# Kernel optimization log

Measured on AMD Instinct MI355X. Metric: run time of the kernel, lower is better.

Reference implementation:

```python
import jax, jax.numpy as jnp
import numpy as np

V, D, DI, S, B, NI = 32000, 1024, 768, 512, 8, 197
EPS = 1e-5

def _ln(x, g, b):
    m = jnp.mean(x, axis=-1, keepdims=True)
    v = jnp.var(x, axis=-1, keepdims=True)
    return (x - m) * jax.lax.rsqrt(v + EPS) * g + b

def _pos_enc(seq_len, d):
    pos = np.arange(seq_len)[:, None].astype(np.float32)
    i = np.arange(0, d, 2).astype(np.float32)
    ang = pos / np.power(10000.0, i / d)
    pe = np.zeros((seq_len, d), dtype=np.float32)
    pe[:, 0::2] = np.sin(ang)
    pe[:, 1::2] = np.cos(ang)
    return jnp.asarray(pe)

def setup_inputs() -> dict:
    key = jax.random.key(0)
    ks = jax.random.split(key, 24)
    def rn(k, shape, scale=0.02):
        return jax.random.normal(k, shape, dtype=jnp.float32) * scale
    return {
        'tokens': jax.random.randint(ks[0], (B, S), 0, V),
        'img_emb': jax.random.normal(ks[1], (B, NI, DI), dtype=jnp.float32),
        'emb_table': rn(ks[2], (V, D), 1.0),
        'Wq1': rn(ks[3], (D, D)), 'bq1': jnp.zeros((D,), jnp.float32),
        'Wk1': rn(ks[4], (D, D)), 'bk1': jnp.zeros((D,), jnp.float32),
        'Wv1': rn(ks[5], (D, D)), 'bv1': jnp.zeros((D,), jnp.float32),
        'g1': jnp.ones((D,), jnp.float32), 'b1': jnp.zeros((D,), jnp.float32),
        'Wq2': rn(ks[6], (D, D)), 'bq2': jnp.zeros((D,), jnp.float32),
        'Wk2': rn(ks[7], (DI, D)), 'bk2': jnp.zeros((D,), jnp.float32),
        'Wv2': rn(ks[8], (DI, D)), 'bv2': jnp.zeros((D,), jnp.float32),
        'g2': jnp.ones((D,), jnp.float32), 'b2': jnp.zeros((D,), jnp.float32),
        'Wp': rn(ks[9], (D, V)), 'bp': jnp.zeros((V,), jnp.float32),
    }

def _forward(tokens, img_emb, emb_table, Wq1, bq1, Wk1, bk1, Wv1, bv1, g1, b1,
             Wq2, bq2, Wk2, bk2, Wv2, bv2, g2, b2, Wp, bp):
    scale = 1.0 / jnp.sqrt(jnp.float32(D))
    x = emb_table[tokens] + _pos_enc(S, D)[None]  # [B,S,D]
    # masked (causal) self-attention
    Q = x @ Wq1 + bq1
    K = x @ Wk1 + bk1
    Vv = x @ Wv1 + bv1
    attn = jnp.einsum('bqd,bkd->bqk', Q, K) * scale
    causal = jnp.tril(jnp.ones((S, S), dtype=bool))
    attn = jnp.where(causal[None], attn, -jnp.inf)
    A = jax.nn.softmax(attn, axis=-1)
    x = _ln(A @ Vv + x, g1, b1)
    # cross-attention over image tokens
    Q2 = x @ Wq2 + bq2
    K2 = img_emb @ Wk2 + bk2
    V2 = img_emb @ Wv2 + bv2
    A2 = jax.nn.softmax(jnp.einsum('bqd,bkd->bqk', Q2, K2) * scale, axis=-1)
    x = _ln(A2 @ V2 + x, g2, b2)
    # vocab projection (note: Decoder.forward never calls self.ff)
    return x @ Wp + bp  # [B,S,V]

def reference(tokens, img_emb, emb_table, Wq1, bq1, Wk1, bk1, Wv1, bv1, g1, b1,
              Wq2, bq2, Wk2, bk2, Wv2, bv2, g2, b2, Wp, bp):
    return _forward(tokens, img_emb, emb_table, Wq1, bq1, Wk1, bk1, Wv1, bv1, g1, b1,
                    Wq2, bq2, Wk2, bk2, Wv2, bv2, g2, b2, Wp, bp)
```

## Files before the change

kernel.cpp:

```cpp
#include <hip/hip_runtime.h>
#include <hip/hip_bf16.h>


#define DEV __device__ __forceinline__

typedef __bf16 bf16x8 __attribute__((ext_vector_type(8)));
typedef float f32x4 __attribute__((ext_vector_type(4)));
typedef unsigned int u32;
typedef __hip_bfloat16 bf16;

DEV void llds16(const void* g, void* l) {
  __builtin_amdgcn_global_load_lds((const __attribute__((address_space(1))) u32*)g,
                                   (__attribute__((address_space(3))) u32*)l, 16, 0, 0);
}

DEV float wredsum(float v){
#pragma unroll
  for (int o = 32; o; o >>= 1) v += __shfl_xor(v, o, 64);
  return v;
}
DEV float wredmax(float v){
#pragma unroll
  for (int o = 32; o; o >>= 1) v = fmaxf(v, __shfl_xor(v, o, 64));
  return v;
}

DEV float b2f(unsigned short x){ return __uint_as_float((u32)x << 16); }

DEV void store_out(float* p, float v){ *p = v; }
DEV void store_out(bf16* p, float v){ *p = __float2bfloat16(v); }

template<typename OutT>
__global__ __launch_bounds__(512, 1) void gemm256_kernel(
    const bf16* __restrict__ A, const bf16* __restrict__ Bt, OutT* __restrict__ C,
    const float* __restrict__ bias, int M, int N, int K, int lda, int ldb, int ldc)
{
  __shared__ alignas(16) char lds[131072];
  const int tid  = threadIdx.x;
  const int wave = tid >> 6, lane = tid & 63;
  const int lo = lane & 15, hi = lane >> 4;
  const int hi2 = hi ^ ((lo >> 1) & 3);
  const int wr = wave >> 2, wc = wave & 3;
  const int koff = (((lane & 3) ^ ((lane >> 3) & 3)) << 3);

  const int nbx = M >> 8;
  const int nwg = nbx * (N >> 8);
  int id = blockIdx.x;
  int g = (nwg & 7) ? id : ((id & 7) * (nwg >> 3) + (id >> 3));
  const int row0 = (g % nbx) * 256, col0 = (g / nbx) * 256;
  const int NT = K >> 5;
  const int srow = lane >> 2;

  auto stageA = [&](int t) {
    char* base = lds + (t & 3) * 32768;
    const int kk = (t << 5) + koff;
#pragma unroll
    for (int j = 0; j < 2; j++) {
      const int seg = j * 8 + wave;
      llds16(A + (long)(row0 + seg * 16 + srow) * lda + kk, base + seg * 1024);
    }
  };
  auto stageB = [&](int t) {
    char* base = lds + (t & 3) * 32768 + 16384;
    const int kk = (t << 5) + koff;
#pragma unroll
    for (int j = 0; j < 2; j++) {
      const int seg = j * 8 + wave;
      llds16(Bt + (long)(col0 + seg * 16 + srow) * ldb + kk, base + seg * 1024);
    }
  };

  f32x4 acc[8][4] = {};

  stageA(0); stageB(0);
  stageA(1); stageB(1);
  stageA(2); stageB(2);
  asm volatile("s_waitcnt vmcnt(8)" ::: "memory");
  __builtin_amdgcn_s_barrier();
  asm volatile("" ::: "memory");

  for (int t = 0; t < NT; t++) {
    char* As = lds + (t & 3) * 32768;
    char* Bs = As + 16384;
    bf16x8 af[4], bfv[4];
#pragma unroll
    for (int m = 0; m < 4; m++)
      af[m] = *(const bf16x8*)(As + ((wr * 128 + m * 16 + lo) << 6) + (hi2 << 4));
#pragma unroll
    for (int n = 0; n < 4; n++)
      bfv[n] = *(const bf16x8*)(Bs + ((wc * 64 + n * 16 + lo) << 6) + (hi2 << 4));
    if (t + 3 < NT) stageA(t + 3);
    __builtin_amdgcn_s_setprio(1);
#pragma unroll
    for (int m = 0; m < 4; m++)
#pragma unroll
      for (int n = 0; n < 4; n++)
        acc[m][n] = __builtin_amdgcn_mfma_f32_16x16x32_bf16(af[m], bfv[n], acc[m][n], 0, 0, 0);
    __builtin_amdgcn_s_setprio(0);
    asm volatile("" ::: "memory");
    __builtin_amdgcn_s_barrier();
    asm volatile("" ::: "memory");
#pragma unroll
    for (int m = 0; m < 4; m++)
      af[m] = *(const bf16x8*)(As + ((wr * 128 + (m + 4) * 16 + lo) << 6) + (hi2 << 4));
    if (t + 3 < NT) stageB(t + 3);
    __builtin_amdgcn_s_setprio(1);
#pragma unroll
    for (int m = 0; m < 4; m++)
#pragma unroll
      for (int n = 0; n < 4; n++)
        acc[m + 4][n] = __builtin_amdgcn_mfma_f32_16x16x32_bf16(af[m], bfv[n], acc[m + 4][n], 0, 0, 0);
    __builtin_amdgcn_s_setprio(0);
    if (t < NT - 3)       asm volatile("s_waitcnt vmcnt(8)" ::: "memory");
    else if (t == NT - 3) asm volatile("s_waitcnt vmcnt(4)" ::: "memory");
    else                  asm volatile("s_waitcnt vmcnt(0)" ::: "memory");
    __builtin_amdgcn_s_barrier();
    asm volatile("" ::: "memory");
  }

#pragma unroll
  for (int m = 0; m < 8; m++) {
    const int r = row0 + wr * 128 + m * 16 + hi * 4;
#pragma unroll
    for (int n = 0; n < 4; n++) {
      const int c = col0 + wc * 64 + n * 16 + lo;
      const float bb = bias ? bias[c] : 0.0f;
#pragma unroll
      for (int j = 0; j < 4; j++)
        store_out(&C[(long)(r + j) * ldc + c], acc[m][n][j] + bb);
    }
  }
}

template<typename OutT>
__global__ __launch_bounds__(256) void gemm_bt_kernel(
    const bf16* __restrict__ A, const bf16* __restrict__ Bt, OutT* __restrict__ C,
    const float* __restrict__ bias, int M, int N, int K,
    int lda, int ldb, int ldc, long sA, long sB, long sC, int tri, int kcausal)
{
  A  += (long)blockIdx.z * sA;
  Bt += (long)blockIdx.z * sB;
  C  += (long)blockIdx.z * sC;
  __shared__ alignas(16) char lds[32768];
  int bx = blockIdx.x, by = blockIdx.y;
  if (tri) { int t = blockIdx.x, i = 0; while (t > i) { t -= i + 1; i++; } bx = i; by = t; }
  const int tid = threadIdx.x;
  const int wave = tid >> 6, lane = tid & 63;
  const int lo = lane & 15, hi = lane >> 4;
  const int hi2 = hi ^ ((lo >> 1) & 3);
  const int wr = wave >> 1, wc = wave & 1;
  const int row0 = bx * 128, col0 = by * 128;
  const int srow  = lane >> 2;
  const int skoff = (((lane & 3) ^ ((lane >> 3) & 3)) << 3);
  const int Keff = kcausal ? (K < row0 + 128 ? K : row0 + 128) : K;
  const int NT = Keff >> 5;

  auto stage = [&](int t) {
    char* base = lds + (t & 1) * 16384;
    const int kk = (t << 5) + skoff;
#pragma unroll
    for (int c = 0; c < 2; ++c) {
      const int seg = c*4 + wave;
      int ra = row0 + seg*16 + srow; ra = ra < M ? ra : M-1;
      llds16(A + (long)ra*lda + kk, base + seg*1024);
      int rb = col0 + seg*16 + srow; rb = rb < N ? rb : N-1;
      llds16(Bt + (long)rb*ldb + kk, base + 8192 + seg*1024);
    }
  };

  f32x4 acc[4][4] = {};

  stage(0);
  asm volatile("s_waitcnt vmcnt(0)" ::: "memory");
  __builtin_amdgcn_s_barrier();
  __builtin_amdgcn_sched_barrier(0);

  for (int t = 0; t < NT; t++) {
    const char* As = lds + (t & 1) * 16384;
    const char* Bs = As + 8192;
    if (t + 1 < NT) stage(t + 1);
    bf16x8 af[4], bfv[4];
#pragma unroll
    for (int m = 0; m < 4; m++)
      af[m] = *(const bf16x8*)(As + ((wr*64 + m*16 + lo) << 6) + (hi2 << 4));
#pragma unroll
    for (int n = 0; n < 4; n++)
      bfv[n] = *(const bf16x8*)(Bs + ((wc*64 + n*16 + lo) << 6) + (hi2 << 4));
    __builtin_amdgcn_s_setprio(1);
#pragma unroll
    for (int m = 0; m < 4; m++)
#pragma unroll
      for (int n = 0; n < 4; n++)
        acc[m][n] = __builtin_amdgcn_mfma_f32_16x16x32_bf16(af[m], bfv[n], acc[m][n], 0, 0, 0);
    __builtin_amdgcn_s_setprio(0);
    __builtin_amdgcn_sched_barrier(0);
    asm volatile("s_waitcnt vmcnt(0)" ::: "memory");
    __builtin_amdgcn_sched_barrier(0);
    __builtin_amdgcn_s_barrier();
    __builtin_amdgcn_sched_barrier(0);
  }

#pragma unroll
  for (int m = 0; m < 4; m++) {
    const int rbase = row0 + wr*64 + m*16 + hi*4;
#pragma unroll
    for (int n = 0; n < 4; n++) {
      const int cc = col0 + wc*64 + n*16 + lo;
      if (cc >= N) continue;
      const float bb = bias ? bias[cc] : 0.0f;
#pragma unroll
      for (int j = 0; j < 4; j++) {
        const int rr = rbase + j;
        if (rr < M) store_out(&C[(long)rr*ldc + cc], acc[m][n][j] + bb);
      }
    }
  }
}

__global__ __launch_bounds__(256) void wprep4_kernel(
    const float* W0, const float* W1, const float* W2, const float* W3,
    bf16* T0, bf16* T1, bf16* T2, bf16* T3, int K, int N)
{
  const int z = blockIdx.z;
  const float* W = z == 0 ? W0 : z == 1 ? W1 : z == 2 ? W2 : W3;
  bf16* T = z == 0 ? T0 : z == 1 ? T1 : z == 2 ? T2 : T3;
  __shared__ bf16 t[32][33];
  const int k0 = blockIdx.x * 32, n0 = blockIdx.y * 32;
  const int tx = threadIdx.x & 31, ty = threadIdx.x >> 5;
#pragma unroll
  for (int i = 0; i < 4; i++)
    t[ty + i*8][tx] = __float2bfloat16(W[(long)(k0 + ty + i*8)*N + n0 + tx]);
  __syncthreads();
#pragma unroll
  for (int i = 0; i < 4; i++)
    T[(long)(n0 + ty + i*8)*K + k0 + tx] = t[tx][ty + i*8];
}

__global__ __launch_bounds__(256) void transpose_pad_kernel(
    const bf16* __restrict__ in, bf16* __restrict__ out,
    int R, int Cc, int inLD, int outLD, long inBatch, long outBatch)
{
  in  += (long)blockIdx.z * inBatch;
  out += (long)blockIdx.z * outBatch;
  __shared__ bf16 t[32][33];
  const int r0 = blockIdx.x * 32, c0 = blockIdx.y * 32;
  const int tx = threadIdx.x & 31, ty = threadIdx.x >> 5;
#pragma unroll
  for (int i = 0; i < 4; i++) {
    const int r = r0 + ty + i*8;
    bf16 v = __float2bfloat16(0.0f);
    if (r < R) v = in[(long)r*inLD + c0 + tx];
    t[ty + i*8][tx] = v;
  }
  __syncthreads();
#pragma unroll
  for (int i = 0; i < 4; i++) {
    const int oc = r0 + tx;
    const int orow = c0 + ty + i*8;
    if (oc < outLD) out[(long)orow*outLD + oc] = t[tx][ty + i*8];
  }
}

__global__ __launch_bounds__(256) void concat_bias_kernel(
    const float* a, const float* b, const float* c, int n1, int n2, int n3, float* out)
{
  const int i = blockIdx.x * 256 + threadIdx.x;
  if (i >= n1 + n2 + n3) return;
  out[i] = i < n1 ? a[i] : (i < n1 + n2 ? b[i - n1] : c[i - n1 - n2]);
}

__global__ __launch_bounds__(256) void embed_kernel(
    const int* __restrict__ tok, const float* __restrict__ tbl,
    bf16* __restrict__ xb)
{
  const int row = blockIdx.x;
  const int s = row & 511;
  const float pos = (float)s;
  const float* te = tbl + (long)tok[row] * 1024;
  const int d0 = threadIdx.x * 4;
  float4 v = *(const float4*)(te + d0);
  float o[4] = {v.x, v.y, v.z, v.w};
#pragma unroll
  for (int k = 0; k < 4; k++) {
    const int d = d0 + k;
    const int i2 = d & ~1;
    const float ang = pos * exp2f((float)i2 * -0.0129762816f);
    o[k] += (d & 1) ? __cosf(ang) : __sinf(ang);
  }
  bf16 ob[4];
#pragma unroll
  for (int k = 0; k < 4; k++) ob[k] = __float2bfloat16(o[k]);
  *(ushort4*)((unsigned short*)xb + (long)row*1024 + d0) = *(ushort4*)ob;
}

__global__ __launch_bounds__(256) void cvt_bf16_kernel(const float* __restrict__ in, bf16* __restrict__ out, long n)
{
  long i = (long)blockIdx.x * blockDim.x + threadIdx.x;
  if (i < n) out[i] = __float2bfloat16(in[i]);
}

__global__ __launch_bounds__(64) void softmax_causal_kernel(
    const float* __restrict__ Sc, bf16* __restrict__ P)
{
  const int row = blockIdx.x;
  const int q = row & 511;
  const float* srow = Sc + (long)row * 512;
  bf16* prow = P + (long)row * 512;
  const int lane = threadIdx.x;
  const float scale = 0.03125f;
  float mx = -1e30f;
  for (int j = lane; j <= q; j += 64) mx = fmaxf(mx, srow[j]);
  mx = wredmax(mx);
  float sum = 0.0f;
  for (int j = lane; j <= q; j += 64) sum += expf((srow[j] - mx) * scale);
  sum = wredsum(sum);
  const float inv = 1.0f / sum;
  for (int j = lane; j < 512; j += 64) {
    float p = (j <= q) ? expf((srow[j] - mx) * scale) * inv : 0.0f;
    prow[j] = __float2bfloat16(p);
  }
}

__global__ __launch_bounds__(64) void softmax_cross_kernel(
    const float* __restrict__ Sc, bf16* __restrict__ P)
{
  const int row = blockIdx.x;
  const float* srow = Sc + (long)row * 224;
  bf16* prow = P + (long)row * 224;
  const int lane = threadIdx.x;
  const float scale = 0.03125f;
  float mx = -1e30f;
  for (int j = lane; j < 197; j += 64) mx = fmaxf(mx, srow[j]);
  mx = wredmax(mx);
  float sum = 0.0f;
  for (int j = lane; j < 197; j += 64) sum += expf((srow[j] - mx) * scale);
  sum = wredsum(sum);
  const float inv = 1.0f / sum;
  for (int j = lane; j < 224; j += 64) {
    float p = (j < 197) ? expf((srow[j] - mx) * scale) * inv : 0.0f;
    prow[j] = __float2bfloat16(p);
  }
}

__global__ __launch_bounds__(256) void add_ln_kernel(
    const bf16* __restrict__ Acc, const bf16* __restrict__ Res,
    const float* __restrict__ g, const float* __restrict__ b,
    bf16* __restrict__ outb)
{
  const int row = blockIdx.x;
  const unsigned short* a = (const unsigned short*)Acc + (long)row * 1024;
  const unsigned short* r = (const unsigned short*)Res + (long)row * 1024;
  const int d0 = threadIdx.x * 4;
  ushort4 av = *(const ushort4*)(a + d0);
  ushort4 rv = *(const ushort4*)(r + d0);
  float vals[4] = { b2f(av.x) + b2f(rv.x), b2f(av.y) + b2f(rv.y),
                    b2f(av.z) + b2f(rv.z), b2f(av.w) + b2f(rv.w) };
  float s = vals[0] + vals[1] + vals[2] + vals[3];
  float ss = vals[0]*vals[0] + vals[1]*vals[1] + vals[2]*vals[2] + vals[3]*vals[3];
  s = wredsum(s); ss = wredsum(ss);
  __shared__ float sh[8];
  const int wave = threadIdx.x >> 6, lane = threadIdx.x & 63;
  if (lane == 0) { sh[wave] = s; sh[wave+4] = ss; }
  __syncthreads();
  s  = sh[0] + sh[1] + sh[2] + sh[3];
  ss = sh[4] + sh[5] + sh[6] + sh[7];
  const float mean = s * (1.0f/1024.0f);
  const float var  = ss * (1.0f/1024.0f) - mean*mean;
  const float inv  = rsqrtf(var + 1e-5f);
  bf16 ob[4];
#pragma unroll
  for (int i = 0; i < 4; i++) {
    const int d = d0 + i;
    ob[i] = __float2bfloat16((vals[i] - mean) * inv * g[d] + b[d]);
  }
  *(ushort4*)((unsigned short*)outb + (long)row*1024 + d0) = *(ushort4*)ob;
}

extern "C" void kernel_launch(void* const* d_in, const int* in_sizes, int n_in,
                              void* d_out, int out_size, void* d_ws, size_t ws_size,
                              hipStream_t stream) {
  const int*   tokens = (const int*)  d_in[0];
  const float* img    = (const float*)d_in[1];
  const float* emb    = (const float*)d_in[2];
  const float* Wq1    = (const float*)d_in[3];
  const float* bq1    = (const float*)d_in[4];
  const float* Wk1    = (const float*)d_in[5];
  const float* bk1    = (const float*)d_in[6];
  const float* Wv1    = (const float*)d_in[7];
  const float* bv1    = (const float*)d_in[8];
  const float* g1     = (const float*)d_in[9];
  const float* b1     = (const float*)d_in[10];
  const float* Wq2    = (const float*)d_in[11];
  const float* bq2    = (const float*)d_in[12];
  const float* Wk2    = (const float*)d_in[13];
  const float* bk2    = (const float*)d_in[14];
  const float* Wv2    = (const float*)d_in[15];
  const float* bv2    = (const float*)d_in[16];
  const float* g2     = (const float*)d_in[17];
  const float* b2     = (const float*)d_in[18];
  const float* Wp     = (const float*)d_in[19];
  const float* bp     = (const float*)d_in[20];
  float* out = (float*)d_out;

  const int B = 8, S = 512, D = 1024, DI = 768, NI = 197, NIP = 224, V = 32000;
  const int M = B * S;
  const int MI = B * NI;

  char* ws = (char*)d_ws;
  size_t off = 0;
  auto alloc = [&](size_t bytes) -> char* {
    char* p = ws + off; off += (bytes + 255) & ~(size_t)255; return p;
  };
  bf16* Wq1t = (bf16*)alloc((size_t)D*D*2);
  bf16* Wk1t = (bf16*)alloc((size_t)D*D*2);
  bf16* Wv1t = (bf16*)alloc((size_t)D*D*2);
  bf16* Wq2t = (bf16*)alloc((size_t)D*D*2);
  bf16* Wk2t = (bf16*)alloc((size_t)D*DI*2);
  bf16* Wv2t = (bf16*)alloc((size_t)D*DI*2);
  bf16* Wpt  = (bf16*)alloc((size_t)V*D*2);
  float* bqkv= (float*)alloc((size_t)3*D*4);
  float* bkv2= (float*)alloc((size_t)2*D*4);
  bf16*  xb  = (bf16*) alloc((size_t)M*D*2);
  bf16*  imgb= (bf16*) alloc((size_t)MI*DI*2);
  bf16*  QKV = (bf16*) alloc((size_t)M*3*D*2);
  bf16*  Vt  = (bf16*) alloc((size_t)M*D*2);
  float* sc1 = (float*)alloc((size_t)B*S*S*4);
  bf16*  P1  = (bf16*) alloc((size_t)B*S*S*2);
  bf16*  ao1 = (bf16*) alloc((size_t)M*D*2);
  bf16*  x2b = (bf16*) alloc((size_t)M*D*2);
  bf16*  Q2  = (bf16*) alloc((size_t)M*D*2);
  bf16*  KV2 = (bf16*) alloc((size_t)MI*2*D*2);
  bf16*  V2t = (bf16*) alloc((size_t)B*D*NIP*2);
  float* sc2 = (float*)alloc((size_t)B*S*NIP*4);
  bf16*  P2  = (bf16*) alloc((size_t)B*S*NIP*2);
  bf16*  ao2 = (bf16*) alloc((size_t)M*D*2);
  bf16*  x3b = (bf16*) alloc((size_t)M*D*2);
  (void)ws_size; (void)in_sizes; (void)n_in; (void)out_size;

  wprep4_kernel<<<dim3(D/32,  D/32, 4), 256, 0, stream>>>(Wq1, Wk1, Wv1, Wq2, Wq1t, Wk1t, Wv1t, Wq2t, D, D);
  wprep4_kernel<<<dim3(DI/32, D/32, 2), 256, 0, stream>>>(Wk2, Wv2, nullptr, nullptr, Wk2t, Wv2t, nullptr, nullptr, DI, D);
  wprep4_kernel<<<dim3(D/32,  V/32, 1), 256, 0, stream>>>(Wp, nullptr, nullptr, nullptr, Wpt, nullptr, nullptr, nullptr, D, V);
  concat_bias_kernel<<<(3*D+255)/256, 256, 0, stream>>>(bq1, bk1, bv1, D, D, D, bqkv);
  concat_bias_kernel<<<(2*D+255)/256, 256, 0, stream>>>(bk2, bv2, nullptr, D, D, 0, bkv2);

  embed_kernel<<<M, 256, 0, stream>>>(tokens, emb, xb);
  {
    long n = (long)MI * DI;
    cvt_bf16_kernel<<<(int)((n + 255)/256), 256, 0, stream>>>(img, imgb, n);
  }

  auto gemmF = [&](const bf16* A, const bf16* Bt, float* C, const float* bias,
                   int m, int n, int k, int lda, int ldb, int ldc,
                   long sA, long sB, long sC, int batch) {
    dim3 g((m+127)/128, (n+127)/128, batch);
    gemm_bt_kernel<float><<<g, 256, 0, stream>>>(A, Bt, C, bias, m, n, k, lda, ldb, ldc, sA, sB, sC, 0, 0);
  };
  auto gemmB = [&](const bf16* A, const bf16* Bt, bf16* C, const float* bias,
                   int m, int n, int k, int lda, int ldb, int ldc,
                   long sA, long sB, long sC, int batch) {
    dim3 g((m+127)/128, (n+127)/128, batch);
    gemm_bt_kernel<bf16><<<g, 256, 0, stream>>>(A, Bt, C, bias, m, n, k, lda, ldb, ldc, sA, sB, sC, 0, 0);
  };

  gemm256_kernel<bf16><<<dim3((M/256)*(3*D/256)), 512, 0, stream>>>(
      xb, Wq1t, QKV, bqkv, M, 3*D, D, D, D, 3*D);
  transpose_pad_kernel<<<dim3(S/32, D/32, B), 256, 0, stream>>>(
      QKV + 2*D, Vt, S, D, 3*D, S, (long)S*3*D, (long)D*S);
  gemm_bt_kernel<float><<<dim3(10, 1, B), 256, 0, stream>>>(
      QKV, QKV + D, sc1, nullptr, S, S, D, 3*D, 3*D, S,
      (long)S*3*D, (long)S*3*D, (long)S*S, 1, 0);
  softmax_causal_kernel<<<M, 64, 0, stream>>>(sc1, P1);
  gemm_bt_kernel<bf16><<<dim3(S/128, D/128, B), 256, 0, stream>>>(
      P1, Vt, ao1, nullptr, S, D, S, S, S, D,
      (long)S*S, (long)D*S, (long)S*D, 0, 1);
  add_ln_kernel<<<M, 256, 0, stream>>>(ao1, xb, g1, b1, x2b);

  gemm256_kernel<bf16><<<dim3((M/256)*(D/256)), 512, 0, stream>>>(
      x2b, Wq2t, Q2, bq2, M, D, D, D, D, D);
  gemmB(imgb, Wk2t, KV2, bkv2, MI, 2*D, DI, DI, DI, 2*D, 0, 0, 0, 1);
  transpose_pad_kernel<<<dim3((NIP+31)/32, D/32, B), 256, 0, stream>>>(
      KV2 + D, V2t, NI, D, 2*D, NIP, (long)NI*2*D, (long)D*NIP);
  gemmF(Q2, KV2, sc2, nullptr, S, NI, D, D, 2*D, NIP, (long)S*D, (long)NI*2*D, (long)S*NIP, B);
  softmax_cross_kernel<<<M, 64, 0, stream>>>(sc2, P2);
  gemmB(P2, V2t, ao2, nullptr, S, D, NIP, NIP, NIP, D, (long)S*NIP, (long)D*NIP, (long)S*D, B);
  add_ln_kernel<<<M, 256, 0, stream>>>(ao2, x2b, g2, b2, x3b);

  gemm256_kernel<float><<<dim3((M/256)*(V/256)), 512, 0, stream>>>(
      x3b, Wpt, out, bp, M, V, D, D, D, V);
}
```

Before: 655.8 us.

## Restructure 256x256 GEMM into BK=64 double-buffered quadrant-staged pipeline

Rewrites the main 256x256 GEMM mainloop to use a K-tile of 64 with two 64KB LDS slots instead of four 32-wide slots. Each tile's loads are split into four quarter stages that are interleaved with four MFMA quadrants, and an 8-way XOR swizzle is used for the 128-byte rows. The aim is to raise the MFMA work done per barrier and per LDS read, and to overlap global-to-LDS traffic more finely with compute. In exchange it adds many more barriers per iteration. The loop also assumes K is a multiple of 128, which could break for other shapes, and the tight LDS double-buffering reuse ordering carries a correctness risk.

```diff
diff --git a/kernel.cpp b/kernel.cpp
--- a/kernel.cpp
+++ b/kernel.cpp
@@ -30,92 +30,104 @@
 DEV void store_out(float* p, float v){ *p = v; }
 DEV void store_out(bf16* p, float v){ *p = __float2bfloat16(v); }
 
+#define SBAR __builtin_amdgcn_sched_barrier(0)
+#define HBAR __builtin_amdgcn_s_barrier()
+#define LGKM0 asm volatile("s_waitcnt lgkmcnt(0)" ::: "memory")
+#define VMC6 asm volatile("s_waitcnt vmcnt(6)" ::: "memory")
+#define VMC0 asm volatile("s_waitcnt vmcnt(0)" ::: "memory")
+
+#define RD_A(slot, mh) do { \
+  _Pragma("unroll") for (int m = 0; m < 4; m++) { \
+    const int r_ = wr*128 + ((mh)*4 + m)*16 + lo; \
+    _Pragma("unroll") for (int ks = 0; ks < 2; ks++) \
+      af[m*2+ks] = *(const bf16x8*)((slot) + r_*128 + ((((ks<<2)|hi) ^ x7) << 4)); \
+  } } while(0)
+#define RD_B(slot, nh) do { \
+  _Pragma("unroll") for (int n = 0; n < 2; n++) { \
+    const int gn_ = (nh)*2 + n; \
+    const int r_ = wc*64 + gn_*16 + lo; \
+    _Pragma("unroll") for (int ks = 0; ks < 2; ks++) \
+      bfv[gn_*2+ks] = *(const bf16x8*)((slot) + 32768 + r_*128 + ((((ks<<2)|hi) ^ x7) << 4)); \
+  } } while(0)
+#define MQ(mh, nh) do { \
+  __builtin_amdgcn_s_setprio(1); \
+  _Pragma("unroll") for (int ks = 0; ks < 2; ks++) \
+  _Pragma("unroll") for (int m = 0; m < 4; m++) \
+  _Pragma("unroll") for (int n = 0; n < 2; n++) \
+    acc[(mh)*4+m][(nh)*2+n] = __builtin_amdgcn_mfma_f32_16x16x32_bf16( \
+        af[m*2+ks], bfv[((nh)*2+n)*2+ks], acc[(mh)*4+m][(nh)*2+n], 0, 0, 0); \
+  __builtin_amdgcn_s_setprio(0); \
+  } while(0)
+
 template<typename OutT>
 __global__ __launch_bounds__(512, 1) void gemm256_kernel(
     const bf16* __restrict__ A, const bf16* __restrict__ Bt, OutT* __restrict__ C,
     const float* __restrict__ bias, int M, int N, int K, int lda, int ldb, int ldc)
 {
   __shared__ alignas(16) char lds[131072];
-  const int tid  = threadIdx.x;
+  const int tid = threadIdx.x;
   const int wave = tid >> 6, lane = tid & 63;
   const int lo = lane & 15, hi = lane >> 4;
-  const int hi2 = hi ^ ((lo >> 1) & 3);
+  const int x7 = lo & 7;
   const int wr = wave >> 2, wc = wave & 3;
-  const int koff = (((lane & 3) ^ ((lane >> 3) & 3)) << 3);
+  const int lr8 = lane >> 3;
+  const int koff = ((lane & 7) ^ lr8) << 3;
 
   const int nbx = M >> 8;
   const int nwg = nbx * (N >> 8);
   int id = blockIdx.x;
   int g = (nwg & 7) ? id : ((id & 7) * (nwg >> 3) + (id >> 3));
   const int row0 = (g % nbx) * 256, col0 = (g / nbx) * 256;
-  const int NT = K >> 5;
-  const int srow = lane >> 2;
-
-  auto stageA = [&](int t) {
-    char* base = lds + (t & 3) * 32768;
-    const int kk = (t << 5) + koff;
+  const int NT2 = K >> 6;
+
+  auto stage = [&](int kind, int t) {
+    if (t >= NT2) return;
+    char* slot = lds + (t & 1) * 65536;
+    const int kk = (t << 6) + koff;
 #pragma unroll
     for (int j = 0; j < 2; j++) {
-      const int seg = j * 8 + wave;
-      llds16(A + (long)(row0 + seg * 16 + srow) * lda + kk, base + seg * 1024);
+      if (kind == 0 || kind == 3) {
+        const int br = ((kind == 3) ? 64 : 0) + j*128 + wave*8;
+        llds16(A + (long)(row0 + br + lr8)*lda + kk, slot + br*128);
+      } else {
+        const int br = ((kind == 2) ? 32 : 0) + (wave&3)*8 + (wave>>2)*64 + j*128;
+        llds16(Bt + (long)(col0 + br + lr8)*ldb + kk, slot + 32768 + br*128);
+      }
     }
   };
-  auto stageB = [&](int t) {
-    char* base = lds + (t & 3) * 32768 + 16384;
-    const int kk = (t << 5) + koff;
-#pragma unroll
-    for (int j = 0; j < 2; j++) {
-      const int seg = j * 8 + wave;
-      llds16(Bt + (long)(col0 + seg * 16 + srow) * ldb + kk, base + seg * 1024);
-    }
-  };
 
   f32x4 acc[8][4] = {};
-
-  stageA(0); stageB(0);
-  stageA(1); stageB(1);
-  stageA(2); stageB(2);
-  asm volatile("s_waitcnt vmcnt(8)" ::: "memory");
-  __builtin_amdgcn_s_barrier();
-  asm volatile("" ::: "memory");
-
-  for (int t = 0; t < NT; t++) {
-    char* As = lds + (t & 3) * 32768;
-    char* Bs = As + 16384;
-    bf16x8 af[4], bfv[4];
-#pragma unroll
-    for (int m = 0; m < 4; m++)
-      af[m] = *(const bf16x8*)(As + ((wr * 128 + m * 16 + lo) << 6) + (hi2 << 4));
-#pragma unroll
-    for (int n = 0; n < 4; n++)
-      bfv[n] = *(const bf16x8*)(Bs + ((wc * 64 + n * 16 + lo) << 6) + (hi2 << 4));
-    if (t + 3 < NT) stageA(t + 3);
-    __builtin_amdgcn_s_setprio(1);
-#pragma unroll
-    for (int m = 0; m < 4; m++)
-#pragma unroll
-      for (int n = 0; n < 4; n++)
-        acc[m][n] = __builtin_amdgcn_mfma_f32_16x16x32_bf16(af[m], bfv[n], acc[m][n], 0, 0, 0);
-    __builtin_amdgcn_s_setprio(0);
-    asm volatile("" ::: "memory");
-    __builtin_amdgcn_s_barrier();
-    asm volatile("" ::: "memory");
-#pragma unroll
-    for (int m = 0; m < 4; m++)
-      af[m] = *(const bf16x8*)(As + ((wr * 128 + (m + 4) * 16 + lo) << 6) + (hi2 << 4));
-    if (t + 3 < NT) stageB(t + 3);
-    __builtin_amdgcn_s_setprio(1);
-#pragma unroll
-    for (int m = 0; m < 4; m++)
-#pragma unroll
-      for (int n = 0; n < 4; n++)
-        acc[m + 4][n] = __builtin_amdgcn_mfma_f32_16x16x32_bf16(af[m], bfv[n], acc[m + 4][n], 0, 0, 0);
-    __builtin_amdgcn_s_setprio(0);
-    if (t < NT - 3)       asm volatile("s_waitcnt vmcnt(8)" ::: "memory");
-    else if (t == NT - 3) asm volatile("s_waitcnt vmcnt(4)" ::: "memory");
-    else                  asm volatile("s_waitcnt vmcnt(0)" ::: "memory");
-    __builtin_amdgcn_s_barrier();
-    asm volatile("" ::: "memory");
+  bf16x8 af[8], bfv[8];
+
+  stage(0,0); stage(1,0); stage(2,0); stage(3,0);
+  stage(0,1); stage(1,1); stage(2,1);
+  VMC6;
+  HBAR; SBAR;
+
+  for (int it = 0; it < (NT2 >> 1); it++) {
+    const int ta = it*2, tb = ta+1;
+    const char* sa = lds;
+    const char* sb = lds + 65536;
+    RD_A(sa, 0); RD_B(sa, 0); SBAR; stage(3, tb); SBAR;
+    HBAR; LGKM0; SBAR; MQ(0, 0); SBAR; HBAR; SBAR;
+    RD_B(sa, 1); SBAR; stage(0, ta+2); SBAR;
+    HBAR; LGKM0; SBAR; MQ(0, 1); SBAR; HBAR; SBAR;
+    RD_A(sa, 1); SBAR; stage(1, ta+2); SBAR;
+    HBAR; LGKM0; SBAR; MQ(1, 0); SBAR; HBAR; SBAR;
+    stage(2, ta+2); SBAR;
+    HBAR; SBAR; MQ(1, 1); SBAR;
+    if (ta+2 < NT2) { VMC6; } else { VMC0; }
+    HBAR; SBAR;
+    RD_A(sb, 0); RD_B(sb, 0); SBAR; stage(3, ta+2); SBAR;
+    HBAR; LGKM0; SBAR; MQ(0, 0); SBAR; HBAR; SBAR;
+    RD_B(sb, 1); SBAR; stage(0, tb+2); SBAR;
+    HBAR; LGKM0; SBAR; MQ(0, 1); SBAR; HBAR; SBAR;
+    RD_A(sb, 1); SBAR; stage(1, tb+2); SBAR;
+    HBAR; LGKM0; SBAR; MQ(1, 0); SBAR; HBAR; SBAR;
+    stage(2, tb+2); SBAR;
+    HBAR; SBAR; MQ(1, 1); SBAR;
+    if (tb+2 < NT2) { VMC6; } else { VMC0; }
+    HBAR; SBAR;
   }
 
 #pragma unroll
@@ -171,9 +183,8 @@
   f32x4 acc[4][4] = {};
 
   stage(0);
-  asm volatile("s_waitcnt vmcnt(0)" ::: "memory");
-  __builtin_amdgcn_s_barrier();
-  __builtin_amdgcn_sched_barrier(0);
+  VMC0;
+  HBAR; SBAR;
 
   for (int t = 0; t < NT; t++) {
     const char* As = lds + (t & 1) * 16384;
@@ -193,11 +204,10 @@
       for (int n = 0; n < 4; n++)
         acc[m][n] = __builtin_amdgcn_mfma_f32_16x16x32_bf16(af[m], bfv[n], acc[m][n], 0, 0, 0);
     __builtin_amdgcn_s_setprio(0);
-    __builtin_amdgcn_sched_barrier(0);
-    asm volatile("s_waitcnt vmcnt(0)" ::: "memory");
-    __builtin_amdgcn_sched_barrier(0);
-    __builtin_amdgcn_s_barrier();
-    __builtin_amdgcn_sched_barrier(0);
+    SBAR;
+    VMC0;
+    SBAR;
+    HBAR; SBAR;
   }
 
 #pragma unroll
```

Result: faster. 636.0 us (median of 3 runs) (-3.0%).

## Replace 256x256 four-stage GEMM with 128x256 double-buffered tile kernel

Applied to the files above, without the earlier changes.

The large GEMM kernel switches from a 256x256 tile with 8 waves and a 4-deep LDS pipeline to a 128x256 tile with 4 waves and double buffering in 48KB of LDS. Launch bounds now allow two workgroups per CU, and the tile count doubles. The intent is better occupancy and more workgroups for the projection GEMMs, covering latency across workgroups instead of through deep prefetch. In exchange, each tile reuses less data, the pipeline is shallower, and every iteration waits for vmcnt(0), which may expose memory latency. Synchronisation macros are also introduced for tidiness.

```diff
diff --git a/kernel.cpp b/kernel.cpp
--- a/kernel.cpp
+++ b/kernel.cpp
@@ -9,6 +9,10 @@
 typedef unsigned int u32;
 typedef __hip_bfloat16 bf16;
 
+#define SBAR __builtin_amdgcn_sched_barrier(0)
+#define HBAR __builtin_amdgcn_s_barrier()
+#define VMC0 asm volatile("s_waitcnt vmcnt(0)" ::: "memory")
+
 DEV void llds16(const void* g, void* l) {
   __builtin_amdgcn_global_load_lds((const __attribute__((address_space(1))) u32*)g,
                                    (__attribute__((address_space(3))) u32*)l, 16, 0, 0);
@@ -31,65 +35,58 @@
 DEV void store_out(bf16* p, float v){ *p = __float2bfloat16(v); }
 
 template<typename OutT>
-__global__ __launch_bounds__(512, 1) void gemm256_kernel(
+__global__ __launch_bounds__(256, 2) void gemm128_kernel(
     const bf16* __restrict__ A, const bf16* __restrict__ Bt, OutT* __restrict__ C,
     const float* __restrict__ bias, int M, int N, int K, int lda, int ldb, int ldc)
 {
-  __shared__ alignas(16) char lds[131072];
-  const int tid  = threadIdx.x;
+  __shared__ alignas(16) char lds[49152];
+  const int tid = threadIdx.x;
   const int wave = tid >> 6, lane = tid & 63;
   const int lo = lane & 15, hi = lane >> 4;
   const int hi2 = hi ^ ((lo >> 1) & 3);
-  const int wr = wave >> 2, wc = wave & 3;
-  const int koff = (((lane & 3) ^ ((lane >> 3) & 3)) << 3);
-
-  const int nbx = M >> 8;
+  const int srow  = lane >> 2;
+  const int skoff = (((lane & 3) ^ ((lane >> 3) & 3)) << 3);
+
+  const int nbx = M >> 7;
   const int nwg = nbx * (N >> 8);
   int id = blockIdx.x;
   int g = (nwg & 7) ? id : ((id & 7) * (nwg >> 3) + (id >> 3));
-  const int row0 = (g % nbx) * 256, col0 = (g / nbx) * 256;
+  const int row0 = (g % nbx) * 128;
+  const int col0 = (g / nbx) * 256;
   const int NT = K >> 5;
-  const int srow = lane >> 2;
-
-  auto stageA = [&](int t) {
-    char* base = lds + (t & 3) * 32768;
-    const int kk = (t << 5) + koff;
+
+  auto stage = [&](int t) {
+    char* slot = lds + (t & 1) * 24576;
+    const int kk = (t << 5) + skoff;
 #pragma unroll
     for (int j = 0; j < 2; j++) {
-      const int seg = j * 8 + wave;
-      llds16(A + (long)(row0 + seg * 16 + srow) * lda + kk, base + seg * 1024);
+      const int seg = wave * 2 + j;
+      llds16(A + (long)(row0 + seg * 16 + srow) * lda + kk, slot + seg * 1024);
+    }
+#pragma unroll
+    for (int j = 0; j < 4; j++) {
+      const int seg = wave * 4 + j;
+      llds16(Bt + (long)(col0 + seg * 16 + srow) * ldb + kk, slot + 8192 + seg * 1024);
     }
   };
-  auto stageB = [&](int t) {
-    char* base = lds + (t & 3) * 32768 + 16384;
-    const int kk = (t << 5) + koff;
-#pragma unroll
-    for (int j = 0; j < 2; j++) {
-      const int seg = j * 8 + wave;
-      llds16(Bt + (long)(col0 + seg * 16 + srow) * ldb + kk, base + seg * 1024);
-    }
-  };
 
   f32x4 acc[8][4] = {};
 
-  stageA(0); stageB(0);
-  stageA(1); stageB(1);
-  stageA(2); stageB(2);
-  asm volatile("s_waitcnt vmcnt(8)" ::: "memory");
-  __builtin_amdgcn_s_barrier();
-  asm volatile("" ::: "memory");
+  stage(0);
+  VMC0;
+  HBAR; SBAR;
 
   for (int t = 0; t < NT; t++) {
-    char* As = lds + (t & 3) * 32768;
-    char* Bs = As + 16384;
+    const char* As = lds + (t & 1) * 24576;
+    const char* Bs = As + 8192;
+    if (t + 1 < NT) stage(t + 1);
     bf16x8 af[4], bfv[4];
 #pragma unroll
-    for (int m = 0; m < 4; m++)
-      af[m] = *(const bf16x8*)(As + ((wr * 128 + m * 16 + lo) << 6) + (hi2 << 4));
-#pragma unroll
     for (int n = 0; n < 4; n++)
-      bfv[n] = *(const bf16x8*)(Bs + ((wc * 64 + n * 16 + lo) << 6) + (hi2 << 4));
-    if (t + 3 < NT) stageA(t + 3);
+      bfv[n] = *(const bf16x8*)(Bs + ((wave * 64 + n * 16 + lo) << 6) + (hi2 << 4));
+#pragma unroll
+    for (int m = 0; m < 4; m++)
+      af[m] = *(const bf16x8*)(As + ((m * 16 + lo) << 6) + (hi2 << 4));
     __builtin_amdgcn_s_setprio(1);
 #pragma unroll
     for (int m = 0; m < 4; m++)
@@ -97,13 +94,9 @@
       for (int n = 0; n < 4; n++)
         acc[m][n] = __builtin_amdgcn_mfma_f32_16x16x32_bf16(af[m], bfv[n], acc[m][n], 0, 0, 0);
     __builtin_amdgcn_s_setprio(0);
-    asm volatile("" ::: "memory");
-    __builtin_amdgcn_s_barrier();
-    asm volatile("" ::: "memory");
-#pragma unroll
-    for (int m = 0; m < 4; m++)
-      af[m] = *(const bf16x8*)(As + ((wr * 128 + (m + 4) * 16 + lo) << 6) + (hi2 << 4));
-    if (t + 3 < NT) stageB(t + 3);
+#pragma unroll
+    for (int m = 0; m < 4; m++)
+      af[m] = *(const bf16x8*)(As + (((m + 4) * 16 + lo) << 6) + (hi2 << 4));
     __builtin_amdgcn_s_setprio(1);
 #pragma unroll
     for (int m = 0; m < 4; m++)
@@ -111,19 +104,18 @@
       for (int n = 0; n < 4; n++)
         acc[m + 4][n] = __builtin_amdgcn_mfma_f32_16x16x32_bf16(af[m], bfv[n], acc[m + 4][n], 0, 0, 0);
     __builtin_amdgcn_s_setprio(0);
-    if (t < NT - 3)       asm volatile("s_waitcnt vmcnt(8)" ::: "memory");
-    else if (t == NT - 3) asm volatile("s_waitcnt vmcnt(4)" ::: "memory");
-    else                  asm volatile("s_waitcnt vmcnt(0)" ::: "memory");
-    __builtin_amdgcn_s_barrier();
-    asm volatile("" ::: "memory");
+    SBAR;
+    VMC0;
+    SBAR;
+    HBAR; SBAR;
   }
 
 #pragma unroll
   for (int m = 0; m < 8; m++) {
-    const int r = row0 + wr * 128 + m * 16 + hi * 4;
+    const int r = row0 + m * 16 + hi * 4;
 #pragma unroll
     for (int n = 0; n < 4; n++) {
-      const int c = col0 + wc * 64 + n * 16 + lo;
+      const int c = col0 + wave * 64 + n * 16 + lo;
       const float bb = bias ? bias[c] : 0.0f;
 #pragma unroll
       for (int j = 0; j < 4; j++)
@@ -171,9 +163,8 @@
   f32x4 acc[4][4] = {};
 
   stage(0);
-  asm volatile("s_waitcnt vmcnt(0)" ::: "memory");
-  __builtin_amdgcn_s_barrier();
-  __builtin_amdgcn_sched_barrier(0);
+  VMC0;
+  HBAR; SBAR;
 
   for (int t = 0; t < NT; t++) {
     const char* As = lds + (t & 1) * 16384;
@@ -193,11 +184,10 @@
       for (int n = 0; n < 4; n++)
         acc[m][n] = __builtin_amdgcn_mfma_f32_16x16x32_bf16(af[m], bfv[n], acc[m][n], 0, 0, 0);
     __builtin_amdgcn_s_setprio(0);
-    __builtin_amdgcn_sched_barrier(0);
-    asm volatile("s_waitcnt vmcnt(0)" ::: "memory");
-    __builtin_amdgcn_sched_barrier(0);
-    __builtin_amdgcn_s_barrier();
-    __builtin_amdgcn_sched_barrier(0);
+    SBAR;
+    VMC0;
+    SBAR;
+    HBAR; SBAR;
   }
 
 #pragma unroll
@@ -462,7 +452,7 @@
     gemm_bt_kernel<bf16><<<g, 256, 0, stream>>>(A, Bt, C, bias, m, n, k, lda, ldb, ldc, sA, sB, sC, 0, 0);
   };
 
-  gemm256_kernel<bf16><<<dim3((M/256)*(3*D/256)), 512, 0, stream>>>(
+  gemm128_kernel<bf16><<<dim3((M/128)*(3*D/256)), 256, 0, stream>>>(
       xb, Wq1t, QKV, bqkv, M, 3*D, D, D, D, 3*D);
   transpose_pad_kernel<<<dim3(S/32, D/32, B), 256, 0, stream>>>(
       QKV + 2*D, Vt, S, D, 3*D, S, (long)S*3*D, (long)D*S);
@@ -475,7 +465,7 @@
       (long)S*S, (long)D*S, (long)S*D, 0, 1);
   add_ln_kernel<<<M, 256, 0, stream>>>(ao1, xb, g1, b1, x2b);
 
-  gemm256_kernel<bf16><<<dim3((M/256)*(D/256)), 512, 0, stream>>>(
+  gemm128_kernel<bf16><<<dim3((M/128)*(D/256)), 256, 0, stream>>>(
       x2b, Wq2t, Q2, bq2, M, D, D, D, D, D);
   gemmB(imgb, Wk2t, KV2, bkv2, MI, 2*D, DI, DI, DI, 2*D, 0, 0, 0, 1);
   transpose_pad_kernel<<<dim3((NIP+31)/32, D/32, B), 256, 0, stream>>>(
@@ -485,6 +475,6 @@
   gemmB(P2, V2t, ao2, nullptr, S, D, NIP, NIP, NIP, D, (long)S*NIP, (long)D*NIP, (long)S*D, B);
   add_ln_kernel<<<M, 256, 0, stream>>>(ao2, x2b, g2, b2, x3b);
 
-  gemm256_kernel<float><<<dim3((M/256)*(V/256)), 512, 0, stream>>>(
+  gemm128_kernel<float><<<dim3((M/128)*(V/256)), 256, 0, stream>>>(
       x3b, Wpt, out, bp, M, V, D, D, D, V);
 }
```

Measured after the change: 679.5 us. 1.04x slower.
